# Kernel tuning notes

Measured on AMD Instinct MI355X. Metric: run time of the kernel, lower is better.

## Reference

```python
import jax, jax.numpy as jnp
import numpy as np

D_MODEL = 1024
N_HEADS = 16
D_HEAD = 64


def setup_inputs() -> dict:
    key = jax.random.key(0)
    ks = jax.random.split(key, 5)
    B, T = 2, 2048
    scale = 1.0 / np.sqrt(D_MODEL)
    x = jax.random.normal(ks[0], (B, T, D_MODEL), dtype=jnp.float32)
    Wq = jax.random.normal(ks[1], (N_HEADS * D_HEAD, D_MODEL), dtype=jnp.float32) * scale
    Wk = jax.random.normal(ks[2], (N_HEADS * D_HEAD, D_MODEL), dtype=jnp.float32) * scale
    Wv = jax.random.normal(ks[3], (N_HEADS * D_HEAD, D_MODEL), dtype=jnp.float32) * scale
    Wo = jax.random.normal(ks[4], (D_MODEL, N_HEADS * D_HEAD), dtype=jnp.float32) * scale
    return {"x": x, "Wq": Wq, "Wk": Wk, "Wv": Wv, "Wo": Wo}


def reference(x, Wq, Wk, Wv, Wo):
    B, T, D = x.shape
    # Linear(y = x @ W.T), then split heads: [B, H, T, d]
    def split_heads(y):
        return y.reshape(B, T, N_HEADS, D_HEAD).transpose(0, 2, 1, 3)
    q = split_heads(x @ Wq.T)
    k = split_heads(x @ Wk.T)
    v = split_heads(x @ Wv.T)
    scale = D_HEAD ** -0.5
    # Materialized [B, H, T, T] scores, as in the original module
    scores = jnp.einsum('bhtd,bhTd->bhtT', q, k) * scale
    attn = jax.nn.softmax(scores, axis=-1)
    y = jnp.einsum('bhtT,bhTd->bhtd', attn, v)
    y = y.transpose(0, 2, 1, 3).reshape(B, T, N_HEADS * D_HEAD)
    return y @ Wo.T
```

## Files before the change

### kernel.cpp

```cpp
#include <hip/hip_runtime.h>
#include <hip/hip_bf16.h>

typedef __attribute__((ext_vector_type(8))) short bf16x8;
typedef __attribute__((ext_vector_type(4))) float f32x4;
typedef unsigned short u16t;

#define DEVINL static __device__ __forceinline__

DEVINL u16t f2bf(float f) {
  union { __hip_bfloat16 h; u16t u; } cv;
  cv.h = __float2bfloat16(f);
  return cv.u;
}

DEVINL u16t f2bf_fast(float f) {
  union { float f; unsigned u; } c;
  c.f = f;
  return (u16t)((c.u + 0x8000u) >> 16);
}

DEVINL void async16(void* lds, const void* g) {
  __builtin_amdgcn_global_load_lds((const __attribute__((address_space(1))) void*)g,
                                   (__attribute__((address_space(3))) void*)lds,
                                   16, 0, 0);
}

__global__ __launch_bounds__(256) void convert_bf16(
    const float* __restrict__ x,  const float* __restrict__ wq,
    const float* __restrict__ wk, const float* __restrict__ wv,
    const float* __restrict__ wo,
    u16t* __restrict__ xb, u16t* __restrict__ wqb, u16t* __restrict__ wkb,
    u16t* __restrict__ wvb, u16t* __restrict__ wob) {
  const int blk = blockIdx.x;
  const float* src; u16t* dst; size_t off;
  if (blk < 4096)      { src = x;  dst = xb;  off = (size_t)blk * 1024; }
  else if (blk < 5120) { src = wq; dst = wqb; off = (size_t)(blk - 4096) * 1024; }
  else if (blk < 6144) { src = wk; dst = wkb; off = (size_t)(blk - 5120) * 1024; }
  else if (blk < 7168) { src = wv; dst = wvb; off = (size_t)(blk - 6144) * 1024; }
  else                 { src = wo; dst = wob; off = (size_t)(blk - 7168) * 1024; }
  const size_t i = off + (size_t)threadIdx.x * 4;
  const float4 v = *(const float4*)&src[i];
  ushort4 r;
  r.x = f2bf(v.x); r.y = f2bf(v.y); r.z = f2bf(v.z); r.w = f2bf(v.w);
  *(ushort4*)&dst[i] = r;
}

template <int MODE>
__global__ __launch_bounds__(256) void gemm_bt(
    const u16t* __restrict__ A, const u16t* __restrict__ B,
    void* __restrict__ C0, void* __restrict__ C1, void* __restrict__ C2,
    int M, int N, int K) {
  __shared__ u16t As[2][128 * 32];
  __shared__ u16t Bs[2][128 * 32];

  const int tid = threadIdx.x;
  const int lane = tid & 63;
  const int w = tid >> 6;
  const int wm = w >> 1, wn = w & 1;
  const int quad = lane >> 4, cl = lane & 15;
  const int m0 = blockIdx.y * 128;
  const int n0 = blockIdx.x * 128;

  const int srow = lane >> 2;
  const int scol = (lane & 3) * 8;

  f32x4 acc[4][4] = {};

  for (int k0 = 0; k0 < K; k0 += 64) {
    __syncthreads();
    #pragma unroll
    for (int p = 0; p < 2; ++p)
      #pragma unroll
      for (int ii = 0; ii < 2; ++ii) {
        const int c = w + ii * 4;
        async16(&As[p][c * 512], &A[(size_t)(m0 + c * 16 + srow) * K + k0 + p * 32 + scol]);
        async16(&Bs[p][c * 512], &B[(size_t)(n0 + c * 16 + srow) * K + k0 + p * 32 + scol]);
      }
    __syncthreads();
    #pragma unroll
    for (int p = 0; p < 2; ++p) {
      bf16x8 af[4], bfr[4];
      #pragma unroll
      for (int i = 0; i < 4; ++i)
        af[i] = *(const bf16x8*)&As[p][(wm * 64 + i * 16 + cl) * 32 + quad * 8];
      #pragma unroll
      for (int j = 0; j < 4; ++j)
        bfr[j] = *(const bf16x8*)&Bs[p][(wn * 64 + j * 16 + cl) * 32 + quad * 8];
      #pragma unroll
      for (int i = 0; i < 4; ++i)
        #pragma unroll
        for (int j = 0; j < 4; ++j)
          acc[i][j] = __builtin_amdgcn_mfma_f32_16x16x32_bf16(af[i], bfr[j], acc[i][j], 0, 0, 0);
    }
  }

  const int nz = n0 >> 10;
  #pragma unroll
  for (int i = 0; i < 4; ++i)
    #pragma unroll
    for (int j = 0; j < 4; ++j) {
      const int mb = m0 + wm * 64 + i * 16 + quad * 4;
      const int n  = n0 + wn * 64 + j * 16 + cl;
      if (MODE == 0) {
        #pragma unroll
        for (int r = 0; r < 4; ++r)
          ((float*)C0)[(size_t)(mb + r) * N + n] = acc[i][j][r];
      } else {
        const int nw = n & 1023, h = nw >> 6, d = nw & 63;
        const int b = mb >> 11, tb = mb & 2047;
        const size_t bh = (size_t)(b * 16 + h);
        if (nz == 2) {
          ushort4 v4;
          v4.x = f2bf(acc[i][j][0]); v4.y = f2bf(acc[i][j][1]);
          v4.z = f2bf(acc[i][j][2]); v4.w = f2bf(acc[i][j][3]);
          const size_t addr = (bh << 17) +
              (size_t)(((d >> 4) * 256 + (tb >> 3)) * 128 + (d & 15) * 8 + (tb & 7));
          *(ushort4*)&((u16t*)C2)[addr] = v4;
        } else if (nz == 1) {
          const size_t basea = (bh << 17) +
              (size_t)(((tb >> 4) * 8 + (d >> 3)) * 128 + (d & 7));
          #pragma unroll
          for (int r = 0; r < 4; ++r)
            ((u16t*)C1)[basea + ((tb & 15) + r) * 8] = f2bf(acc[i][j][r]);
        } else {
          #pragma unroll
          for (int r = 0; r < 4; ++r)
            ((u16t*)C0)[(bh * 2048 + tb + r) * 64 + d] =
                f2bf(acc[i][j][r] * 0.18033688011112043f);
        }
      }
    }
}

__global__ __launch_bounds__(256) void flash_attn(
    const u16t* __restrict__ Q, const u16t* __restrict__ Kt,
    const u16t* __restrict__ Vt, u16t* __restrict__ Y) {
  __shared__ u16t Ps[4 * 16 * 136];

  const int tid = threadIdx.x;
  const int lane = tid & 63;
  const int w = tid >> 6;
  const int quad = lane >> 4, cl = lane & 15;
  const int bh = blockIdx.y;
  const int q0 = blockIdx.x * 64;
  const u16t* Kb = Kt + ((size_t)bh << 17);
  const u16t* Vb = Vt + ((size_t)bh << 17);

  bf16x8 aq[2];
  #pragma unroll
  for (int ks = 0; ks < 2; ++ks)
    aq[ks] = *(const bf16x8*)&Q[((size_t)bh * 2048 + q0 + w * 16 + cl) * 64 + ks * 32 + quad * 8];

  f32x4 o[4] = {};
  float lsum[4] = {0.f, 0.f, 0.f, 0.f};

  u16t* Pw = &Ps[w * 16 * 136];

  for (int jt = 0; jt < 16; ++jt) {
    const int j0 = jt * 128;

    f32x4 s[8] = {};
    #pragma unroll
    for (int ks = 0; ks < 2; ++ks) {
      bf16x8 kf[8];
      #pragma unroll
      for (int js = 0; js < 8; ++js)
        kf[js] = *(const bf16x8*)&Kb[(size_t)((((j0 >> 4) + js) * 8 + ks * 4) * 128) + lane * 8];
      #pragma unroll
      for (int js = 0; js < 8; ++js)
        s[js] = __builtin_amdgcn_mfma_f32_16x16x32_bf16(aq[ks], kf[js], s[js], 0, 0, 0);
    }

    #pragma unroll
    for (int js = 0; js < 8; ++js)
      #pragma unroll
      for (int r = 0; r < 4; ++r) {
        const float p = __builtin_exp2f(s[js][r]);
        lsum[r] += p;
        Pw[(quad * 4 + r) * 136 + js * 16 + cl] = f2bf_fast(p);
      }

    #pragma unroll
    for (int ks = 0; ks < 4; ++ks) {
      const bf16x8 ap = *(const bf16x8*)&Pw[cl * 136 + ks * 32 + quad * 8];
      bf16x8 vf[4];
      #pragma unroll
      for (int ds = 0; ds < 4; ++ds)
        vf[ds] = *(const bf16x8*)&Vb[(size_t)((ds * 256 + (j0 >> 3) + ks * 4) * 128) + lane * 8];
      #pragma unroll
      for (int ds = 0; ds < 4; ++ds)
        o[ds] = __builtin_amdgcn_mfma_f32_16x16x32_bf16(ap, vf[ds], o[ds], 0, 0, 0);
    }
  }

  #pragma unroll
  for (int r = 0; r < 4; ++r) {
    #pragma unroll
    for (int msk = 1; msk < 16; msk <<= 1) lsum[r] += __shfl_xor(lsum[r], msk, 64);
  }

  const int b = bh >> 4, h = bh & 15;
  #pragma unroll
  for (int ds = 0; ds < 4; ++ds)
    #pragma unroll
    for (int r = 0; r < 4; ++r) {
      const int t = q0 + w * 16 + quad * 4 + r;
      const int d = ds * 16 + cl;
      Y[((size_t)b * 2048 + t) * 1024 + h * 64 + d] = f2bf(o[ds][r] / lsum[r]);
    }
}

extern "C" void kernel_launch(void* const* d_in, const int* in_sizes, int n_in,
                              void* d_out, int out_size, void* d_ws, size_t ws_size,
                              hipStream_t stream) {
  (void)in_sizes; (void)n_in; (void)out_size; (void)ws_size;
  const float* x  = (const float*)d_in[0];
  const float* Wq = (const float*)d_in[1];
  const float* Wk = (const float*)d_in[2];
  const float* Wv = (const float*)d_in[3];
  const float* Wo = (const float*)d_in[4];

  char* ws = (char*)d_ws;
  const size_t MB = 1024 * 1024;
  u16t* xb  = (u16t*)(ws);
  u16t* Wqb = (u16t*)(ws + 8 * MB);
  u16t* Wkb = (u16t*)(ws + 10 * MB);
  u16t* Wvb = (u16t*)(ws + 12 * MB);
  u16t* Wob = (u16t*)(ws + 14 * MB);
  u16t* Qw  = (u16t*)(ws + 16 * MB);
  u16t* Ktw = (u16t*)(ws + 24 * MB);
  u16t* Vtw = (u16t*)(ws + 32 * MB);
  u16t* Yw  = xb;

  convert_bf16<<<8192, 256, 0, stream>>>(x, Wq, Wk, Wv, Wo, xb, Wqb, Wkb, Wvb, Wob);
  gemm_bt<1><<<dim3(24, 32), 256, 0, stream>>>(
      xb, Wqb, Qw, Ktw, Vtw, 4096, 3072, 1024);
  flash_attn<<<dim3(32, 32), 256, 0, stream>>>(Qw, Ktw, Vtw, Yw);
  gemm_bt<0><<<dim3(8, 32), 256, 0, stream>>>(
      Yw, Wob, d_out, d_out, d_out, 4096, 1024, 1024);
}
```

Before: 215.4 us.

## Prefetch K fragments in attention, widen output GEMM, use fast bf16 rounding

The attention loop now loads the next tile's first K half-fragments while the current tile's score MFMAs run, and interleaves loads of the second half with compute to hide global latency. The attention kernel also gets a min-blocks occupancy hint. The output projection GEMM runs with 8 waves per block, each owning a 32-row slice, to raise the number of waves in flight. All bf16 conversions switch to a cheap add-and-shift rounding that does not handle NaN or ties exactly like the library routine.

```diff
diff --git a/kernel.cpp b/kernel.cpp
--- a/kernel.cpp
+++ b/kernel.cpp
@@ -6,12 +6,6 @@
 typedef unsigned short u16t;
 
 #define DEVINL static __device__ __forceinline__
-
-DEVINL u16t f2bf(float f) {
-  union { __hip_bfloat16 h; u16t u; } cv;
-  cv.h = __float2bfloat16(f);
-  return cv.u;
-}
 
 DEVINL u16t f2bf_fast(float f) {
   union { float f; unsigned u; } c;
@@ -41,15 +35,18 @@
   const size_t i = off + (size_t)threadIdx.x * 4;
   const float4 v = *(const float4*)&src[i];
   ushort4 r;
-  r.x = f2bf(v.x); r.y = f2bf(v.y); r.z = f2bf(v.z); r.w = f2bf(v.w);
+  r.x = f2bf_fast(v.x); r.y = f2bf_fast(v.y);
+  r.z = f2bf_fast(v.z); r.w = f2bf_fast(v.w);
   *(ushort4*)&dst[i] = r;
 }
 
-template <int MODE>
-__global__ __launch_bounds__(256) void gemm_bt(
+template <int MODE, int NW>
+__global__ __launch_bounds__(NW * 64) void gemm_bt(
     const u16t* __restrict__ A, const u16t* __restrict__ B,
     void* __restrict__ C0, void* __restrict__ C1, void* __restrict__ C2,
     int M, int N, int K) {
+  constexpr int MW = (NW == 4) ? 64 : 32;
+  constexpr int MI = MW / 16;
   __shared__ u16t As[2][128 * 32];
   __shared__ u16t Bs[2][128 * 32];
 
@@ -64,30 +61,31 @@
   const int srow = lane >> 2;
   const int scol = (lane & 3) * 8;
 
-  f32x4 acc[4][4] = {};
+  f32x4 acc[MI][4] = {};
 
   for (int k0 = 0; k0 < K; k0 += 64) {
     __syncthreads();
     #pragma unroll
-    for (int p = 0; p < 2; ++p)
-      #pragma unroll
-      for (int ii = 0; ii < 2; ++ii) {
-        const int c = w + ii * 4;
+    for (int p = 0; p < 2; ++p) {
+      #pragma unroll
+      for (int ii = 0; ii < 8 / NW; ++ii) {
+        const int c = w + ii * NW;
         async16(&As[p][c * 512], &A[(size_t)(m0 + c * 16 + srow) * K + k0 + p * 32 + scol]);
         async16(&Bs[p][c * 512], &B[(size_t)(n0 + c * 16 + srow) * K + k0 + p * 32 + scol]);
       }
+    }
     __syncthreads();
     #pragma unroll
     for (int p = 0; p < 2; ++p) {
-      bf16x8 af[4], bfr[4];
-      #pragma unroll
-      for (int i = 0; i < 4; ++i)
-        af[i] = *(const bf16x8*)&As[p][(wm * 64 + i * 16 + cl) * 32 + quad * 8];
+      bf16x8 af[MI], bfr[4];
+      #pragma unroll
+      for (int i = 0; i < MI; ++i)
+        af[i] = *(const bf16x8*)&As[p][(wm * MW + i * 16 + cl) * 32 + quad * 8];
       #pragma unroll
       for (int j = 0; j < 4; ++j)
         bfr[j] = *(const bf16x8*)&Bs[p][(wn * 64 + j * 16 + cl) * 32 + quad * 8];
       #pragma unroll
-      for (int i = 0; i < 4; ++i)
+      for (int i = 0; i < MI; ++i)
         #pragma unroll
         for (int j = 0; j < 4; ++j)
           acc[i][j] = __builtin_amdgcn_mfma_f32_16x16x32_bf16(af[i], bfr[j], acc[i][j], 0, 0, 0);
@@ -96,10 +94,10 @@
 
   const int nz = n0 >> 10;
   #pragma unroll
-  for (int i = 0; i < 4; ++i)
+  for (int i = 0; i < MI; ++i)
     #pragma unroll
     for (int j = 0; j < 4; ++j) {
-      const int mb = m0 + wm * 64 + i * 16 + quad * 4;
+      const int mb = m0 + wm * MW + i * 16 + quad * 4;
       const int n  = n0 + wn * 64 + j * 16 + cl;
       if (MODE == 0) {
         #pragma unroll
@@ -111,8 +109,8 @@
         const size_t bh = (size_t)(b * 16 + h);
         if (nz == 2) {
           ushort4 v4;
-          v4.x = f2bf(acc[i][j][0]); v4.y = f2bf(acc[i][j][1]);
-          v4.z = f2bf(acc[i][j][2]); v4.w = f2bf(acc[i][j][3]);
+          v4.x = f2bf_fast(acc[i][j][0]); v4.y = f2bf_fast(acc[i][j][1]);
+          v4.z = f2bf_fast(acc[i][j][2]); v4.w = f2bf_fast(acc[i][j][3]);
           const size_t addr = (bh << 17) +
               (size_t)(((d >> 4) * 256 + (tb >> 3)) * 128 + (d & 15) * 8 + (tb & 7));
           *(ushort4*)&((u16t*)C2)[addr] = v4;
@@ -121,18 +119,18 @@
               (size_t)(((tb >> 4) * 8 + (d >> 3)) * 128 + (d & 7));
           #pragma unroll
           for (int r = 0; r < 4; ++r)
-            ((u16t*)C1)[basea + ((tb & 15) + r) * 8] = f2bf(acc[i][j][r]);
+            ((u16t*)C1)[basea + ((tb & 15) + r) * 8] = f2bf_fast(acc[i][j][r]);
         } else {
           #pragma unroll
           for (int r = 0; r < 4; ++r)
             ((u16t*)C0)[(bh * 2048 + tb + r) * 64 + d] =
-                f2bf(acc[i][j][r] * 0.18033688011112043f);
+                f2bf_fast(acc[i][j][r] * 0.18033688011112043f);
         }
       }
     }
 }
 
-__global__ __launch_bounds__(256) void flash_attn(
+__global__ __launch_bounds__(256, 4) void flash_attn(
     const u16t* __restrict__ Q, const u16t* __restrict__ Kt,
     const u16t* __restrict__ Vt, u16t* __restrict__ Y) {
   __shared__ u16t Ps[4 * 16 * 136];
@@ -156,20 +154,36 @@
 
   u16t* Pw = &Ps[w * 16 * 136];
 
+  #define KFRAG(jt, ks, js) \
+    (*(const bf16x8*)&Kb[(size_t)((((jt) * 8 + (js)) * 8 + (ks) * 4) * 128) + lane * 8])
+
+  bf16x8 kn[8];
+  #pragma unroll
+  for (int js = 0; js < 8; ++js) kn[js] = KFRAG(0, 0, js);
+
   for (int jt = 0; jt < 16; ++jt) {
     const int j0 = jt * 128;
-
     f32x4 s[8] = {};
-    #pragma unroll
-    for (int ks = 0; ks < 2; ++ks) {
-      bf16x8 kf[8];
-      #pragma unroll
-      for (int js = 0; js < 8; ++js)
-        kf[js] = *(const bf16x8*)&Kb[(size_t)((((j0 >> 4) + js) * 8 + ks * 4) * 128) + lane * 8];
-      #pragma unroll
-      for (int js = 0; js < 8; ++js)
-        s[js] = __builtin_amdgcn_mfma_f32_16x16x32_bf16(aq[ks], kf[js], s[js], 0, 0, 0);
-    }
+
+    bf16x8 k1a[4];
+    #pragma unroll
+    for (int js = 0; js < 4; ++js) k1a[js] = KFRAG(jt, 1, js);
+    #pragma unroll
+    for (int js = 0; js < 8; ++js)
+      s[js] = __builtin_amdgcn_mfma_f32_16x16x32_bf16(aq[0], kn[js], s[js], 0, 0, 0);
+    bf16x8 k1b[4];
+    #pragma unroll
+    for (int js = 0; js < 4; ++js) k1b[js] = KFRAG(jt, 1, js + 4);
+    #pragma unroll
+    for (int js = 0; js < 4; ++js)
+      s[js] = __builtin_amdgcn_mfma_f32_16x16x32_bf16(aq[1], k1a[js], s[js], 0, 0, 0);
+    #pragma unroll
+    for (int js = 0; js < 4; ++js)
+      s[js + 4] = __builtin_amdgcn_mfma_f32_16x16x32_bf16(aq[1], k1b[js], s[js + 4], 0, 0, 0);
+
+    const int jn = (jt + 1) & 15;
+    #pragma unroll
+    for (int js = 0; js < 8; ++js) kn[js] = KFRAG(jn, 0, js);
 
     #pragma unroll
     for (int js = 0; js < 8; ++js)
@@ -192,6 +206,7 @@
         o[ds] = __builtin_amdgcn_mfma_f32_16x16x32_bf16(ap, vf[ds], o[ds], 0, 0, 0);
     }
   }
+  #undef KFRAG
 
   #pragma unroll
   for (int r = 0; r < 4; ++r) {
@@ -206,7 +221,7 @@
     for (int r = 0; r < 4; ++r) {
       const int t = q0 + w * 16 + quad * 4 + r;
       const int d = ds * 16 + cl;
-      Y[((size_t)b * 2048 + t) * 1024 + h * 64 + d] = f2bf(o[ds][r] / lsum[r]);
+      Y[((size_t)b * 2048 + t) * 1024 + h * 64 + d] = f2bf_fast(o[ds][r] / lsum[r]);
     }
 }
 
@@ -233,9 +248,9 @@
   u16t* Yw  = xb;
 
   convert_bf16<<<8192, 256, 0, stream>>>(x, Wq, Wk, Wv, Wo, xb, Wqb, Wkb, Wvb, Wob);
-  gemm_bt<1><<<dim3(24, 32), 256, 0, stream>>>(
+  gemm_bt<1, 4><<<dim3(24, 32), 256, 0, stream>>>(
       xb, Wqb, Qw, Ktw, Vtw, 4096, 3072, 1024);
   flash_attn<<<dim3(32, 32), 256, 0, stream>>>(Qw, Ktw, Vtw, Yw);
-  gemm_bt<0><<<dim3(8, 32), 256, 0, stream>>>(
+  gemm_bt<0, 8><<<dim3(8, 32), 512, 0, stream>>>(
       Yw, Wob, d_out, d_out, d_out, 4096, 1024, 1024);
 }
```

Result: slower. 229.7 us (+6.6%).
